# Optimization experiments

Measured on AMD Instinct MI355X. Metric: run time of the kernel, lower is better.

Reference implementation:

```python
import jax, jax.numpy as jnp
import numpy as np

N_NODES = 100000
N_EDGES = 600000
C_IN, C_HID, C_OUT = 256, 128, 128
LN_EPS = 1e-5
NEG_SLOPE = 0.01  # nn.LeakyReLU default


def setup_inputs() -> dict:
    key = jax.random.key(0)
    ks = jax.random.split(key, 9)
    x = jax.random.normal(ks[0], (N_NODES, C_IN), dtype=jnp.float32)
    x_struct = jax.random.normal(ks[1], (1,), dtype=jnp.float32)  # unused by forward
    x_e = jax.random.normal(ks[2], (1,), dtype=jnp.float32)       # unused by forward
    edge_index = jax.random.randint(ks[3], (2, N_EDGES), 0, N_NODES, dtype=jnp.int64)
    W1 = jax.random.normal(ks[4], (C_IN, C_HID), dtype=jnp.float32) / np.sqrt(C_IN)
    b1 = jnp.zeros((C_HID,), dtype=jnp.float32)
    gamma = jnp.ones((C_HID,), dtype=jnp.float32)
    beta = jnp.zeros((C_HID,), dtype=jnp.float32)
    W2 = jax.random.normal(ks[5], (C_HID, C_OUT), dtype=jnp.float32) / np.sqrt(C_HID)
    b2 = jnp.zeros((C_OUT,), dtype=jnp.float32)
    return {"x": x, "x_struct": x_struct, "x_e": x_e, "edge_index": edge_index,
            "W1": W1, "b1": b1, "gamma": gamma, "beta": beta, "W2": W2, "b2": b2}


def reference(x, x_struct, x_e, edge_index, W1, b1, gamma, beta, W2, b2):
    # dropout is identity in eval mode
    h = jax.nn.leaky_relu(x @ W1 + b1, negative_slope=NEG_SLOPE)  # [N, H]
    # LayerNorm over last dim
    mu = jnp.mean(h, axis=-1, keepdims=True)
    var = jnp.mean(jnp.square(h - mu), axis=-1, keepdims=True)
    h = (h - mu) * jax.lax.rsqrt(var + LN_EPS) * gamma + beta
    # gather source-node features, scatter-min into destination nodes
    src, dst = edge_index[0], edge_index[1]
    msgs = h[src]                                                 # [E, H]
    agg = jax.ops.segment_min(msgs, dst, num_segments=N_NODES)   # empty -> +inf
    counts = jax.ops.segment_sum(jnp.ones((msgs.shape[0],), dtype=jnp.float32),
                                 dst, num_segments=N_NODES)
    agg = jnp.where(counts[:, None] > 0, agg, 0.0)               # PyG fills empty with 0
    return agg @ W2 + b2                                          # [N, C_OUT]
```

## Files before the change

### kernel.cpp

```cpp
#include <hip/hip_runtime.h>
#include <hip/hip_bf16.h>
#include <cstdint>

#define N_NODES 100000
#define N_EDGES 600000
#define C_IN    256
#define C_HID   128
#define C_OUT   128
#define LN_EPS  1e-5f
#define NEG_SLOPE 0.01f

#define NSCAN_BLOCKS 391

typedef float f32x4 __attribute__((ext_vector_type(4)));
typedef __attribute__((ext_vector_type(8))) short frag_ab;

__device__ __forceinline__ void split2(float f, ushort& h, ushort& l) {
    unsigned u = __float_as_uint(f);
    h = (ushort)(u >> 16);
    float d = f - __uint_as_float(u & 0xFFFF0000u);
    l = (ushort)(__float_as_uint(d) >> 16);
}

__device__ __forceinline__ void split8(const float4& p, const float4& q,
                                       frag_ab& hi, frag_ab& lo) {
    ushort h, l;
    split2(p.x, h, l); hi[0] = (short)h; lo[0] = (short)l;
    split2(p.y, h, l); hi[1] = (short)h; lo[1] = (short)l;
    split2(p.z, h, l); hi[2] = (short)h; lo[2] = (short)l;
    split2(p.w, h, l); hi[3] = (short)h; lo[3] = (short)l;
    split2(q.x, h, l); hi[4] = (short)h; lo[4] = (short)l;
    split2(q.y, h, l); hi[5] = (short)h; lo[5] = (short)l;
    split2(q.z, h, l); hi[6] = (short)h; lo[6] = (short)l;
    split2(q.w, h, l); hi[7] = (short)h; lo[7] = (short)l;
}

__global__ __launch_bounds__(256) void presplit_w_kernel(
    const float* __restrict__ W1, const float* __restrict__ W2,
    ushort* __restrict__ w1s, ushort* __restrict__ w2s)
{
    int tg = blockIdx.x * 256 + threadIdx.x;
    const float* W; ushort* out; int t;
    if (tg < 4096)      { W = W1; out = w1s; t = tg; }
    else if (tg < 6144) { W = W2; out = w2s; t = tg - 4096; }
    else return;

    int lane = t & 63;
    int ks   = (t >> 6) & 3;
    int nf   = (t >> 8) & 7;
    int kc   = t >> 11;
    int k0   = kc * 128 + ks * 32 + (lane >> 4) * 8;
    int n    = nf * 16 + (lane & 15);

    frag_ab hi, lo;
    #pragma unroll
    for (int j = 0; j < 8; ++j) {
        ushort h, l;
        split2(W[(size_t)(k0 + j) * 128 + n], h, l);
        hi[j] = (short)h; lo[j] = (short)l;
    }
    size_t fbase = (size_t)((kc * 32 + nf * 4 + ks) * 2) * 64 + lane;
    ((frag_ab*)out)[fbase]      = hi;
    ((frag_ab*)out)[fbase + 64] = lo;
}

__global__ __launch_bounds__(256) void zero_kernel(int* __restrict__ p, int n) {
    int i = blockIdx.x * 256 + threadIdx.x;
    if (i < n) p[i] = 0;
}

__global__ __launch_bounds__(256) void hist_kernel(const int* __restrict__ ei,
                                                   int* __restrict__ deg) {
    int t = blockIdx.x * 256 + threadIdx.x;
    if (t < N_EDGES) atomicAdd(&deg[ei[N_EDGES + t]], 1);
}

__global__ __launch_bounds__(256) void block_sum_kernel(const int* __restrict__ deg,
                                                        int* __restrict__ bsum) {
    __shared__ int s[256];
    int i = blockIdx.x * 256 + threadIdx.x;
    s[threadIdx.x] = (i < N_NODES) ? deg[i] : 0;
    __syncthreads();
    #pragma unroll
    for (int o = 128; o > 0; o >>= 1) {
        if (threadIdx.x < o) s[threadIdx.x] += s[threadIdx.x + o];
        __syncthreads();
    }
    if (threadIdx.x == 0) bsum[blockIdx.x] = s[0];
}

__global__ __launch_bounds__(512) void scan_bsum_kernel(const int* __restrict__ bsum,
                                                        int* __restrict__ bpre,
                                                        int* __restrict__ offsets) {
    __shared__ int bufA[512], bufB[512];
    int t = threadIdx.x;
    int v = (t < NSCAN_BLOCKS) ? bsum[t] : 0;
    bufA[t] = v;
    __syncthreads();
    int* src = bufA; int* dst = bufB;
    #pragma unroll
    for (int o = 1; o < 512; o <<= 1) {
        dst[t] = src[t] + ((t >= o) ? src[t - o] : 0);
        __syncthreads();
        int* tmp = src; src = dst; dst = tmp;
    }
    if (t < NSCAN_BLOCKS) bpre[t] = src[t] - v;
    if (t == 0) offsets[N_NODES] = N_EDGES;
}

__global__ __launch_bounds__(256) void scan_block_kernel(const int* __restrict__ deg,
                                                         const int* __restrict__ bpre,
                                                         int* __restrict__ offsets) {
    __shared__ int bufA[256], bufB[256];
    int t = threadIdx.x;
    int i = blockIdx.x * 256 + t;
    int v = (i < N_NODES) ? deg[i] : 0;
    bufA[t] = v;
    __syncthreads();
    int* src = bufA; int* dst = bufB;
    #pragma unroll
    for (int o = 1; o < 256; o <<= 1) {
        dst[t] = src[t] + ((t >= o) ? src[t - o] : 0);
        __syncthreads();
        int* tmp = src; src = dst; dst = tmp;
    }
    if (i < N_NODES) offsets[i] = bpre[blockIdx.x] + src[t] - v;
}

__global__ __launch_bounds__(256) void csr_scatter_kernel(const int* __restrict__ ei,
                                                          const int* __restrict__ offsets,
                                                          int* __restrict__ cursor,
                                                          int* __restrict__ csr) {
    int t = blockIdx.x * 256 + threadIdx.x;
    if (t < N_EDGES) {
        int src = ei[t];
        int dst = ei[N_EDGES + t];
        int pos = atomicAdd(&cursor[dst], 1);
        csr[offsets[dst] + pos] = src;
    }
}

__global__ __launch_bounds__(256, 3) void gemm1_ln_mfma_kernel(
    const float* __restrict__ x, const ushort* __restrict__ w1s,
    const float* __restrict__ b1, const float* __restrict__ gamma,
    const float* __restrict__ beta, float* __restrict__ h)
{
    const int tid  = threadIdx.x;
    const int lane = tid & 63;
    const int wv   = tid >> 6;
    const int r16  = lane & 15;
    const int g    = lane >> 4;
    const int row0 = blockIdx.x * 128;

    const frag_ab* B1 = (const frag_ab*)w1s;

    f32x4 acc[2][8];
    #pragma unroll
    for (int mf = 0; mf < 2; ++mf)
        #pragma unroll
        for (int nf = 0; nf < 8; ++nf)
            acc[mf][nf] = (f32x4){0.f, 0.f, 0.f, 0.f};

    float b1v[8], gv[8], bv[8];
    #pragma unroll
    for (int nf = 0; nf < 8; ++nf) {
        int cidx = nf * 16 + r16;
        b1v[nf] = b1[cidx]; gv[nf] = gamma[cidx]; bv[nf] = beta[cidx];
    }

    #pragma unroll
    for (int kc = 0; kc < 2; ++kc) {
        float4 araw[2][4][2];
        #pragma unroll
        for (int mf = 0; mf < 2; ++mf) {
            int r_a = row0 + wv * 32 + mf * 16 + r16;
            r_a = (r_a < N_NODES) ? r_a : (N_NODES - 1);
            const float* xp = x + (size_t)r_a * C_IN + kc * 128 + g * 8;
            #pragma unroll
            for (int ks = 0; ks < 4; ++ks) {
                araw[mf][ks][0] = *(const float4*)(xp + ks * 32);
                araw[mf][ks][1] = *(const float4*)(xp + ks * 32 + 4);
            }
        }

        #pragma unroll
        for (int ks = 0; ks < 4; ++ks) {
            frag_ab aHi[2], aLo[2];
            split8(araw[0][ks][0], araw[0][ks][1], aHi[0], aLo[0]);
            split8(araw[1][ks][0], araw[1][ks][1], aHi[1], aLo[1]);
            const int fb = (kc * 32 + ks) * 128 + lane;
            #pragma unroll
            for (int nf = 0; nf < 8; ++nf) {
                frag_ab bHi = B1[fb + nf * 512];
                frag_ab bLo = B1[fb + nf * 512 + 64];
                acc[0][nf] = __builtin_amdgcn_mfma_f32_16x16x32_bf16(aHi[0], bHi, acc[0][nf], 0, 0, 0);
                acc[0][nf] = __builtin_amdgcn_mfma_f32_16x16x32_bf16(aLo[0], bHi, acc[0][nf], 0, 0, 0);
                acc[0][nf] = __builtin_amdgcn_mfma_f32_16x16x32_bf16(aHi[0], bLo, acc[0][nf], 0, 0, 0);
                acc[1][nf] = __builtin_amdgcn_mfma_f32_16x16x32_bf16(aHi[1], bHi, acc[1][nf], 0, 0, 0);
                acc[1][nf] = __builtin_amdgcn_mfma_f32_16x16x32_bf16(aLo[1], bHi, acc[1][nf], 0, 0, 0);
                acc[1][nf] = __builtin_amdgcn_mfma_f32_16x16x32_bf16(aHi[1], bLo, acc[1][nf], 0, 0, 0);
            }
        }
    }

    #pragma unroll
    for (int mf = 0; mf < 2; ++mf)
        #pragma unroll
        for (int nf = 0; nf < 8; ++nf)
            #pragma unroll
            for (int rg = 0; rg < 4; ++rg) {
                float v = acc[mf][nf][rg] + b1v[nf];
                acc[mf][nf][rg] = (v > 0.f) ? v : NEG_SLOPE * v;
            }

    #pragma unroll
    for (int mf = 0; mf < 2; ++mf) {
        #pragma unroll
        for (int rg = 0; rg < 4; ++rg) {
            float s = 0.f, ss = 0.f;
            #pragma unroll
            for (int nf = 0; nf < 8; ++nf) {
                float v = acc[mf][nf][rg];
                s += v; ss += v * v;
            }
            #pragma unroll
            for (int m = 1; m < 16; m <<= 1) {
                s  += __shfl_xor(s,  m, 64);
                ss += __shfl_xor(ss, m, 64);
            }
            float mu   = s * (1.f / C_HID);
            float var  = ss * (1.f / C_HID) - mu * mu;
            float rstd = rsqrtf(var + LN_EPS);
            int row = row0 + wv * 32 + mf * 16 + (g << 2) + rg;
            if (row < N_NODES) {
                #pragma unroll
                for (int nf = 0; nf < 8; ++nf) {
                    float o = (acc[mf][nf][rg] - mu) * rstd * gv[nf] + bv[nf];
                    h[(size_t)row * C_HID + nf * 16 + r16] = o;
                }
            }
        }
    }
}

__global__ __launch_bounds__(256) void gather_min_kernel(
    const float* __restrict__ h, const int* __restrict__ offsets,
    const int* __restrict__ csr, float* __restrict__ agg)
{
    const int lane = threadIdx.x & 63;
    const int row  = blockIdx.x * 4 + (threadIdx.x >> 6);
    if (row >= N_NODES) return;

    const int beg = offsets[row];
    const int end = offsets[row + 1];

    float m0 = INFINITY, m1 = INFINITY;

    for (int j0 = beg; j0 < end; j0 += 64) {
        const int cnt = min(64, end - j0);
        int idx = (lane < cnt) ? csr[j0 + lane] : 0;
        for (int k = 0; k < cnt; k += 4) {
            int s0 = __shfl(idx, k + 0);
            int s1 = __shfl(idx, k + 1);
            int s2 = __shfl(idx, k + 2);
            int s3 = __shfl(idx, k + 3);
            float2 v0 = ((const float2*)(h + (size_t)s0 * C_HID))[lane];
            float2 v1 = make_float2(INFINITY, INFINITY);
            float2 v2 = make_float2(INFINITY, INFINITY);
            float2 v3 = make_float2(INFINITY, INFINITY);
            if (k + 1 < cnt) v1 = ((const float2*)(h + (size_t)s1 * C_HID))[lane];
            if (k + 2 < cnt) v2 = ((const float2*)(h + (size_t)s2 * C_HID))[lane];
            if (k + 3 < cnt) v3 = ((const float2*)(h + (size_t)s3 * C_HID))[lane];
            m0 = fminf(fminf(m0, v0.x), fminf(fminf(v1.x, v2.x), v3.x));
            m1 = fminf(fminf(m1, v0.y), fminf(fminf(v1.y, v2.y), v3.y));
        }
    }

    if (m0 == INFINITY) m0 = 0.f;
    if (m1 == INFINITY) m1 = 0.f;
    ((float2*)(agg + (size_t)row * C_HID))[lane] = make_float2(m0, m1);
}

__global__ __launch_bounds__(256, 3) void gemm2_mfma_kernel(
    const float* __restrict__ agg, const ushort* __restrict__ w2s,
    const float* __restrict__ b2, float* __restrict__ out)
{
    const int tid  = threadIdx.x;
    const int lane = tid & 63;
    const int wv   = tid >> 6;
    const int r16  = lane & 15;
    const int g    = lane >> 4;
    const int row0 = blockIdx.x * 128;

    const frag_ab* B2 = (const frag_ab*)w2s;

    f32x4 acc[2][8];
    #pragma unroll
    for (int mf = 0; mf < 2; ++mf)
        #pragma unroll
        for (int nf = 0; nf < 8; ++nf)
            acc[mf][nf] = (f32x4){0.f, 0.f, 0.f, 0.f};

    float b2v[8];
    #pragma unroll
    for (int nf = 0; nf < 8; ++nf) b2v[nf] = b2[nf * 16 + r16];

    float4 araw[2][4][2];
    #pragma unroll
    for (int mf = 0; mf < 2; ++mf) {
        int r_a = row0 + wv * 32 + mf * 16 + r16;
        r_a = (r_a < N_NODES) ? r_a : (N_NODES - 1);
        const float* ap = agg + (size_t)r_a * C_HID + g * 8;
        #pragma unroll
        for (int ks = 0; ks < 4; ++ks) {
            araw[mf][ks][0] = *(const float4*)(ap + ks * 32);
            araw[mf][ks][1] = *(const float4*)(ap + ks * 32 + 4);
        }
    }

    #pragma unroll
    for (int ks = 0; ks < 4; ++ks) {
        frag_ab aHi[2], aLo[2];
        split8(araw[0][ks][0], araw[0][ks][1], aHi[0], aLo[0]);
        split8(araw[1][ks][0], araw[1][ks][1], aHi[1], aLo[1]);
        const int fb = ks * 128 + lane;
        #pragma unroll
        for (int nf = 0; nf < 8; ++nf) {
            frag_ab bHi = B2[fb + nf * 512];
            frag_ab bLo = B2[fb + nf * 512 + 64];
            acc[0][nf] = __builtin_amdgcn_mfma_f32_16x16x32_bf16(aHi[0], bHi, acc[0][nf], 0, 0, 0);
            acc[0][nf] = __builtin_amdgcn_mfma_f32_16x16x32_bf16(aLo[0], bHi, acc[0][nf], 0, 0, 0);
            acc[0][nf] = __builtin_amdgcn_mfma_f32_16x16x32_bf16(aHi[0], bLo, acc[0][nf], 0, 0, 0);
            acc[1][nf] = __builtin_amdgcn_mfma_f32_16x16x32_bf16(aHi[1], bHi, acc[1][nf], 0, 0, 0);
            acc[1][nf] = __builtin_amdgcn_mfma_f32_16x16x32_bf16(aLo[1], bHi, acc[1][nf], 0, 0, 0);
            acc[1][nf] = __builtin_amdgcn_mfma_f32_16x16x32_bf16(aHi[1], bLo, acc[1][nf], 0, 0, 0);
        }
    }

    #pragma unroll
    for (int mf = 0; mf < 2; ++mf) {
        #pragma unroll
        for (int rg = 0; rg < 4; ++rg) {
            int row = row0 + wv * 32 + mf * 16 + (g << 2) + rg;
            if (row < N_NODES) {
                #pragma unroll
                for (int nf = 0; nf < 8; ++nf)
                    out[(size_t)row * C_OUT + nf * 16 + r16] = acc[mf][nf][rg] + b2v[nf];
            }
        }
    }
}

extern "C" void kernel_launch(void* const* d_in, const int* in_sizes, int n_in,
                              void* d_out, int out_size, void* d_ws, size_t ws_size,
                              hipStream_t stream)
{
    const float* x     = (const float*)d_in[0];
    const int*   ei    = (const int*)d_in[3];
    const float* W1    = (const float*)d_in[4];
    const float* b1    = (const float*)d_in[5];
    const float* gamma = (const float*)d_in[6];
    const float* beta  = (const float*)d_in[7];
    const float* W2    = (const float*)d_in[8];
    const float* b2    = (const float*)d_in[9];
    float*       out   = (float*)d_out;

    char* p = (char*)d_ws;
    float*  h       = (float*)p;           p += (size_t)N_NODES * C_HID * 4;
    float*  agg     = (float*)p;           p += (size_t)N_NODES * C_HID * 4;
    int*    deg     = (int*)p;             p += 400000;
    int*    cursor  = (int*)p;             p += 400000;
    int*    offsets = (int*)p;             p += 400016;
    int*    bsum    = (int*)p;             p += 1600;
    int*    bpre    = (int*)p;             p += 1600;
    int*    csr     = (int*)p;             p += (size_t)N_EDGES * 4;
    ushort* w1s     = (ushort*)p;          p += 131072;
    ushort* w2s     = (ushort*)p;

    const int grid_e    = (N_EDGES + 255) / 256;
    const int grid_gemm = (N_NODES + 127) / 128;

    presplit_w_kernel<<<24, 256, 0, stream>>>(W1, W2, w1s, w2s);
    zero_kernel<<<(2 * N_NODES + 255) / 256, 256, 0, stream>>>(deg, 2 * N_NODES);
    hist_kernel<<<grid_e, 256, 0, stream>>>(ei, deg);
    block_sum_kernel<<<NSCAN_BLOCKS, 256, 0, stream>>>(deg, bsum);
    scan_bsum_kernel<<<1, 512, 0, stream>>>(bsum, bpre, offsets);
    scan_block_kernel<<<NSCAN_BLOCKS, 256, 0, stream>>>(deg, bpre, offsets);
    csr_scatter_kernel<<<grid_e, 256, 0, stream>>>(ei, offsets, cursor, csr);
    gemm1_ln_mfma_kernel<<<grid_gemm, 256, 0, stream>>>(x, w1s, b1, gamma, beta, h);
    gather_min_kernel<<<(N_NODES + 3) / 4, 256, 0, stream>>>(h, offsets, csr, agg);
    gemm2_mfma_kernel<<<grid_gemm, 256, 0, stream>>>(agg, w2s, b2, out);
}
```

Measured before the change: 386.6 us.

## Stage GEMM weight fragments in LDS with double-buffered async loads

```diff
diff --git a/kernel.cpp b/kernel.cpp
--- a/kernel.cpp
+++ b/kernel.cpp
@@ -35,11 +35,19 @@
     split2(q.w, h, l); hi[7] = (short)h; lo[7] = (short)l;
 }
 
-__global__ __launch_bounds__(256) void presplit_w_kernel(
+__device__ __forceinline__ void gload_lds16(const void* g, void* l) {
+    __builtin_amdgcn_global_load_lds(
+        (const __attribute__((address_space(1))) unsigned int*)g,
+        (__attribute__((address_space(3))) unsigned int*)l, 16, 0, 0);
+}
+
+__global__ __launch_bounds__(256) void setup_kernel(
     const float* __restrict__ W1, const float* __restrict__ W2,
-    ushort* __restrict__ w1s, ushort* __restrict__ w2s)
+    ushort* __restrict__ w1s, ushort* __restrict__ w2s, int* __restrict__ dz)
 {
     int tg = blockIdx.x * 256 + threadIdx.x;
+    if (tg < 2 * N_NODES) dz[tg] = 0;
+
     const float* W; ushort* out; int t;
     if (tg < 4096)      { W = W1; out = w1s; t = tg; }
     else if (tg < 6144) { W = W2; out = w2s; t = tg - 4096; }
@@ -59,14 +67,9 @@
         split2(W[(size_t)(k0 + j) * 128 + n], h, l);
         hi[j] = (short)h; lo[j] = (short)l;
     }
-    size_t fbase = (size_t)((kc * 32 + nf * 4 + ks) * 2) * 64 + lane;
-    ((frag_ab*)out)[fbase]      = hi;
-    ((frag_ab*)out)[fbase + 64] = lo;
-}
-
-__global__ __launch_bounds__(256) void zero_kernel(int* __restrict__ p, int n) {
-    int i = blockIdx.x * 256 + threadIdx.x;
-    if (i < n) p[i] = 0;
+    size_t fi = ((size_t)(kc * 4 + ks) * 16 + nf * 2) * 64 + lane;
+    ((frag_ab*)out)[fi]      = hi;
+    ((frag_ab*)out)[fi + 64] = lo;
 }
 
 __global__ __launch_bounds__(256) void hist_kernel(const int* __restrict__ ei,
@@ -145,14 +148,23 @@
     const float* __restrict__ b1, const float* __restrict__ gamma,
     const float* __restrict__ beta, float* __restrict__ h)
 {
+    __shared__ ushort sB[2][8192];
+
     const int tid  = threadIdx.x;
     const int lane = tid & 63;
     const int wv   = tid >> 6;
     const int r16  = lane & 15;
-    const int g    = lane >> 4;
+    const int quad = lane >> 4;
     const int row0 = blockIdx.x * 128;
 
-    const frag_ab* B1 = (const frag_ab*)w1s;
+    int rA[2];
+    const float* xrow[2];
+    #pragma unroll
+    for (int mf = 0; mf < 2; ++mf) {
+        int r = row0 + wv * 32 + mf * 16 + r16;
+        rA[mf] = (r < N_NODES) ? r : (N_NODES - 1);
+        xrow[mf] = x + (size_t)rA[mf] * C_IN;
+    }
 
     f32x4 acc[2][8];
     #pragma unroll
@@ -160,47 +172,62 @@
         #pragma unroll
         for (int nf = 0; nf < 8; ++nf)
             acc[mf][nf] = (f32x4){0.f, 0.f, 0.f, 0.f};
+
+    float4 a[2][2][2];
+
+    auto ISSUE = [&](int g) {
+        const int par = g & 1;
+        const int col0 = (g >> 2) * 128 + (g & 3) * 32 + quad * 8;
+        #pragma unroll
+        for (int mf = 0; mf < 2; ++mf) {
+            const float* xp = xrow[mf] + col0;
+            a[par][mf][0] = *(const float4*)(xp);
+            a[par][mf][1] = *(const float4*)(xp + 4);
+        }
+        const char* gsrc = (const char*)w1s + g * 16384 + wv * 4096 + lane * 16;
+        char* ldst = (char*)&sB[par][0] + wv * 4096;
+        #pragma unroll
+        for (int it = 0; it < 4; ++it)
+            gload_lds16(gsrc + it * 1024, ldst + it * 1024);
+    };
+
+    ISSUE(0);
+    #pragma unroll
+    for (int g = 0; g < 8; ++g) {
+        if (g < 7) {
+            ISSUE(g + 1);
+            asm volatile("s_waitcnt vmcnt(8)" ::: "memory");
+        } else {
+            asm volatile("s_waitcnt vmcnt(0)" ::: "memory");
+        }
+        __builtin_amdgcn_s_barrier();
+        __builtin_amdgcn_sched_barrier(0);
+
+        const int par = g & 1;
+        frag_ab aHi[2], aLo[2];
+        split8(a[par][0][0], a[par][0][1], aHi[0], aLo[0]);
+        split8(a[par][1][0], a[par][1][1], aHi[1], aLo[1]);
+        const char* bb = (const char*)&sB[par][0] + lane * 16;
+        #pragma unroll
+        for (int nf = 0; nf < 8; ++nf) {
+            frag_ab bHi = *(const frag_ab*)(bb + nf * 2048);
+            frag_ab bLo = *(const frag_ab*)(bb + nf * 2048 + 1024);
+            acc[0][nf] = __builtin_amdgcn_mfma_f32_16x16x32_bf16(aHi[0], bHi, acc[0][nf], 0, 0, 0);
+            acc[0][nf] = __builtin_amdgcn_mfma_f32_16x16x32_bf16(aLo[0], bHi, acc[0][nf], 0, 0, 0);
+            acc[0][nf] = __builtin_amdgcn_mfma_f32_16x16x32_bf16(aHi[0], bLo, acc[0][nf], 0, 0, 0);
+            acc[1][nf] = __builtin_amdgcn_mfma_f32_16x16x32_bf16(aHi[1], bHi, acc[1][nf], 0, 0, 0);
+            acc[1][nf] = __builtin_amdgcn_mfma_f32_16x16x32_bf16(aLo[1], bHi, acc[1][nf], 0, 0, 0);
+            acc[1][nf] = __builtin_amdgcn_mfma_f32_16x16x32_bf16(aHi[1], bLo, acc[1][nf], 0, 0, 0);
+        }
+        __builtin_amdgcn_sched_barrier(0);
+        __builtin_amdgcn_s_barrier();
+    }
 
     float b1v[8], gv[8], bv[8];
     #pragma unroll
     for (int nf = 0; nf < 8; ++nf) {
         int cidx = nf * 16 + r16;
         b1v[nf] = b1[cidx]; gv[nf] = gamma[cidx]; bv[nf] = beta[cidx];
-    }
-
-    #pragma unroll
-    for (int kc = 0; kc < 2; ++kc) {
-        float4 araw[2][4][2];
-        #pragma unroll
-        for (int mf = 0; mf < 2; ++mf) {
-            int r_a = row0 + wv * 32 + mf * 16 + r16;
-            r_a = (r_a < N_NODES) ? r_a : (N_NODES - 1);
-            const float* xp = x + (size_t)r_a * C_IN + kc * 128 + g * 8;
-            #pragma unroll
-            for (int ks = 0; ks < 4; ++ks) {
-                araw[mf][ks][0] = *(const float4*)(xp + ks * 32);
-                araw[mf][ks][1] = *(const float4*)(xp + ks * 32 + 4);
-            }
-        }
-
-        #pragma unroll
-        for (int ks = 0; ks < 4; ++ks) {
-            frag_ab aHi[2], aLo[2];
-            split8(araw[0][ks][0], araw[0][ks][1], aHi[0], aLo[0]);
-            split8(araw[1][ks][0], araw[1][ks][1], aHi[1], aLo[1]);
-            const int fb = (kc * 32 + ks) * 128 + lane;
-            #pragma unroll
-            for (int nf = 0; nf < 8; ++nf) {
-                frag_ab bHi = B1[fb + nf * 512];
-                frag_ab bLo = B1[fb + nf * 512 + 64];
-                acc[0][nf] = __builtin_amdgcn_mfma_f32_16x16x32_bf16(aHi[0], bHi, acc[0][nf], 0, 0, 0);
-                acc[0][nf] = __builtin_amdgcn_mfma_f32_16x16x32_bf16(aLo[0], bHi, acc[0][nf], 0, 0, 0);
-                acc[0][nf] = __builtin_amdgcn_mfma_f32_16x16x32_bf16(aHi[0], bLo, acc[0][nf], 0, 0, 0);
-                acc[1][nf] = __builtin_amdgcn_mfma_f32_16x16x32_bf16(aHi[1], bHi, acc[1][nf], 0, 0, 0);
-                acc[1][nf] = __builtin_amdgcn_mfma_f32_16x16x32_bf16(aLo[1], bHi, acc[1][nf], 0, 0, 0);
-                acc[1][nf] = __builtin_amdgcn_mfma_f32_16x16x32_bf16(aHi[1], bLo, acc[1][nf], 0, 0, 0);
-            }
-        }
     }
 
     #pragma unroll
@@ -231,7 +258,7 @@
             float mu   = s * (1.f / C_HID);
             float var  = ss * (1.f / C_HID) - mu * mu;
             float rstd = rsqrtf(var + LN_EPS);
-            int row = row0 + wv * 32 + mf * 16 + (g << 2) + rg;
+            int row = row0 + wv * 32 + mf * 16 + (quad << 2) + rg;
             if (row < N_NODES) {
                 #pragma unroll
                 for (int nf = 0; nf < 8; ++nf) {
@@ -285,14 +312,22 @@
     const float* __restrict__ agg, const ushort* __restrict__ w2s,
     const float* __restrict__ b2, float* __restrict__ out)
 {
+    __shared__ ushort sB[2][8192];
+
     const int tid  = threadIdx.x;
     const int lane = tid & 63;
     const int wv   = tid >> 6;
     const int r16  = lane & 15;
-    const int g    = lane >> 4;
+    const int quad = lane >> 4;
     const int row0 = blockIdx.x * 128;
 
-    const frag_ab* B2 = (const frag_ab*)w2s;
+    const float* arow[2];
+    #pragma unroll
+    for (int mf = 0; mf < 2; ++mf) {
+        int r = row0 + wv * 32 + mf * 16 + r16;
+        r = (r < N_NODES) ? r : (N_NODES - 1);
+        arow[mf] = agg + (size_t)r * C_HID;
+    }
 
     f32x4 acc[2][8];
     #pragma unroll
@@ -301,33 +336,45 @@
         for (int nf = 0; nf < 8; ++nf)
             acc[mf][nf] = (f32x4){0.f, 0.f, 0.f, 0.f};
 
-    float b2v[8];
-    #pragma unroll
-    for (int nf = 0; nf < 8; ++nf) b2v[nf] = b2[nf * 16 + r16];
-
-    float4 araw[2][4][2];
-    #pragma unroll
-    for (int mf = 0; mf < 2; ++mf) {
-        int r_a = row0 + wv * 32 + mf * 16 + r16;
-        r_a = (r_a < N_NODES) ? r_a : (N_NODES - 1);
-        const float* ap = agg + (size_t)r_a * C_HID + g * 8;
-        #pragma unroll
-        for (int ks = 0; ks < 4; ++ks) {
-            araw[mf][ks][0] = *(const float4*)(ap + ks * 32);
-            araw[mf][ks][1] = *(const float4*)(ap + ks * 32 + 4);
-        }
-    }
-
-    #pragma unroll
-    for (int ks = 0; ks < 4; ++ks) {
+    float4 a[2][2][2];
+
+    auto ISSUE = [&](int g) {
+        const int par = g & 1;
+        const int col0 = g * 32 + quad * 8;
+        #pragma unroll
+        for (int mf = 0; mf < 2; ++mf) {
+            const float* ap = arow[mf] + col0;
+            a[par][mf][0] = *(const float4*)(ap);
+            a[par][mf][1] = *(const float4*)(ap + 4);
+        }
+        const char* gsrc = (const char*)w2s + g * 16384 + wv * 4096 + lane * 16;
+        char* ldst = (char*)&sB[par][0] + wv * 4096;
+        #pragma unroll
+        for (int it = 0; it < 4; ++it)
+            gload_lds16(gsrc + it * 1024, ldst + it * 1024);
+    };
+
+    ISSUE(0);
+    #pragma unroll
+    for (int g = 0; g < 4; ++g) {
+        if (g < 3) {
+            ISSUE(g + 1);
+            asm volatile("s_waitcnt vmcnt(8)" ::: "memory");
+        } else {
+            asm volatile("s_waitcnt vmcnt(0)" ::: "memory");
+        }
+        __builtin_amdgcn_s_barrier();
+        __builtin_amdgcn_sched_barrier(0);
+
+        const int par = g & 1;
         frag_ab aHi[2], aLo[2];
-        split8(araw[0][ks][0], araw[0][ks][1], aHi[0], aLo[0]);
-        split8(araw[1][ks][0], araw[1][ks][1], aHi[1], aLo[1]);
-        const int fb = ks * 128 + lane;
+        split8(a[par][0][0], a[par][0][1], aHi[0], aLo[0]);
+        split8(a[par][1][0], a[par][1][1], aHi[1], aLo[1]);
+        const char* bb = (const char*)&sB[par][0] + lane * 16;
         #pragma unroll
         for (int nf = 0; nf < 8; ++nf) {
-            frag_ab bHi = B2[fb + nf * 512];
-            frag_ab bLo = B2[fb + nf * 512 + 64];
+            frag_ab bHi = *(const frag_ab*)(bb + nf * 2048);
+            frag_ab bLo = *(const frag_ab*)(bb + nf * 2048 + 1024);
             acc[0][nf] = __builtin_amdgcn_mfma_f32_16x16x32_bf16(aHi[0], bHi, acc[0][nf], 0, 0, 0);
             acc[0][nf] = __builtin_amdgcn_mfma_f32_16x16x32_bf16(aLo[0], bHi, acc[0][nf], 0, 0, 0);
             acc[0][nf] = __builtin_amdgcn_mfma_f32_16x16x32_bf16(aHi[0], bLo, acc[0][nf], 0, 0, 0);
@@ -335,13 +382,19 @@
             acc[1][nf] = __builtin_amdgcn_mfma_f32_16x16x32_bf16(aLo[1], bHi, acc[1][nf], 0, 0, 0);
             acc[1][nf] = __builtin_amdgcn_mfma_f32_16x16x32_bf16(aHi[1], bLo, acc[1][nf], 0, 0, 0);
         }
-    }
+        __builtin_amdgcn_sched_barrier(0);
+        __builtin_amdgcn_s_barrier();
+    }
+
+    float b2v[8];
+    #pragma unroll
+    for (int nf = 0; nf < 8; ++nf) b2v[nf] = b2[nf * 16 + r16];
 
     #pragma unroll
     for (int mf = 0; mf < 2; ++mf) {
         #pragma unroll
         for (int rg = 0; rg < 4; ++rg) {
-            int row = row0 + wv * 32 + mf * 16 + (g << 2) + rg;
+            int row = row0 + wv * 32 + mf * 16 + (quad << 2) + rg;
             if (row < N_NODES) {
                 #pragma unroll
                 for (int nf = 0; nf < 8; ++nf)
@@ -380,8 +433,7 @@
     const int grid_e    = (N_EDGES + 255) / 256;
     const int grid_gemm = (N_NODES + 127) / 128;
 
-    presplit_w_kernel<<<24, 256, 0, stream>>>(W1, W2, w1s, w2s);
-    zero_kernel<<<(2 * N_NODES + 255) / 256, 256, 0, stream>>>(deg, 2 * N_NODES);
+    setup_kernel<<<grid_gemm, 256, 0, stream>>>(W1, W2, w1s, w2s, deg);
     hist_kernel<<<grid_e, 256, 0, stream>>>(ei, deg);
     block_sum_kernel<<<NSCAN_BLOCKS, 256, 0, stream>>>(deg, bsum);
     scan_bsum_kernel<<<1, 512, 0, stream>>>(bsum, bpre, offsets);
```

New measurement: 342.3 us. 1.13x faster.
